# Kernel optimization log

Measured on AMD Instinct MI355X. Metric: run time of the kernel, lower is better.

## Reference

```python
import jax, jax.numpy as jnp
import numpy as np

NUM_CLASSES = 54
EPSILON = 0.001
IMPORTANT = [1, 3, 5, 7, 11, 13, 17, 19, 23, 29, 31, 37]
BATCH = 2_000_000


def setup_inputs() -> dict:
    key = jax.random.key(0)
    k1, k2 = jax.random.split(key)
    logits = jax.random.normal(k1, (BATCH, NUM_CLASSES), dtype=jnp.float32)
    target = jax.random.randint(k2, (BATCH,), 0, NUM_CLASSES, dtype=jnp.int64 if jax.config.read('jax_enable_x64') else jnp.int32)
    important_mask = jnp.zeros((NUM_CLASSES,), dtype=bool).at[jnp.array(IMPORTANT)].set(True)
    return {"logits": logits, "target": target, "important_mask": important_mask}


def reference(logits, target, important_mask):
    # softmax over classes
    sm = jax.nn.softmax(logits, axis=1)                     # [B, C]
    pred = jnp.argmax(sm, axis=1)                           # [B]
    # vectorized membership test (replaces the per-sample .item() loop)
    keep = important_mask[pred] | important_mask[target]    # [B]
    # NLLLoss only reads the target column of log(adjusted_softmax):
    #   kept sample   -> softmax[i, target[i]]
    #   ignored sample-> 1 - (C-1)*epsilon  (constant)
    p_target = jnp.take_along_axis(sm, target[:, None], axis=1)[:, 0]  # [B]
    target_prob = 1.0 - (NUM_CLASSES - 1) * EPSILON
    adj = jnp.where(keep, p_target, target_prob)
    loss = -jnp.mean(jnp.log(adj))
    return loss
```

## Files before the change

### kernel.cpp

```cpp
#include <hip/hip_runtime.h>

#define NCLS 54
#define ROWS 64
#define BATCH_N 2000000
#define NTILES (BATCH_N / ROWS)
#define DATA_FLOATS (ROWS * NCLS)
#define TILE_DWORDS (DATA_FLOATS + ROWS)
#define NBLOCKS 1280

#define IMP_MASK ((1ULL << 1) | (1ULL << 3) | (1ULL << 5) | (1ULL << 7) |   \
                  (1ULL << 11) | (1ULL << 13) | (1ULL << 17) | (1ULL << 19) | \
                  (1ULL << 23) | (1ULL << 29) | (1ULL << 31) | (1ULL << 37))

typedef __attribute__((address_space(3))) unsigned int lds_u32;
typedef const __attribute__((address_space(1))) unsigned int glob_u32;

__global__ __launch_bounds__(64) void loss_main(
    const float* __restrict__ logits,
    const int* __restrict__ target,
    float* __restrict__ partial) {
    __shared__ __align__(16) unsigned int tile[2][TILE_DWORDS];

    const int tid = threadIdx.x;

    auto prefetch = [&](int t, int buf) {
        const glob_u32* g = (const glob_u32*)(logits + (size_t)t * DATA_FLOATS);
#pragma unroll
        for (int c = 0; c < 13; ++c) {
            __builtin_amdgcn_global_load_lds(
                g + c * 256 + tid * 4, (lds_u32*)(&tile[buf][c * 256]), 16, 0, 0);
        }
        if (tid < 32) {
            __builtin_amdgcn_global_load_lds(
                g + 13 * 256 + tid * 4, (lds_u32*)(&tile[buf][13 * 256]), 16, 0, 0);
        }
        const glob_u32* gt = (const glob_u32*)(target + (size_t)t * ROWS);
        if (tid < 16) {
            __builtin_amdgcn_global_load_lds(
                gt + tid * 4, (lds_u32*)(&tile[buf][DATA_FLOATS]), 16, 0, 0);
        }
    };

    int t = blockIdx.x;
    prefetch(t, 0);
    prefetch(t + NBLOCKS, 1);

    float acc = 0.0f;
    int buf = 0;
    for (; t < NTILES; t += NBLOCKS) {
        if (t + NBLOCKS < NTILES) {
            asm volatile("s_waitcnt vmcnt(15)" ::: "memory");
        } else {
            asm volatile("s_waitcnt vmcnt(0)" ::: "memory");
        }

        const float* rv = (const float*)&tile[buf][tid * NCLS];
        float v[NCLS];
#pragma unroll
        for (int j = 0; j < NCLS / 2; ++j) {
            float2 t2 = reinterpret_cast<const float2*>(rv)[j];
            v[2 * j] = t2.x;
            v[2 * j + 1] = t2.y;
        }
        const int tg = ((const int*)&tile[buf][DATA_FLOATS])[tid];
        const float vt = rv[tg];

        asm volatile("s_waitcnt lgkmcnt(0)" ::: "memory");
        if (t + 2 * NBLOCKS < NTILES) prefetch(t + 2 * NBLOCKS, buf);

        float w[27];
#pragma unroll
        for (int j = 0; j < 27; ++j) w[j] = fmaxf(v[j], v[j + 27]);
#pragma unroll
        for (int j = 0; j < 13; ++j) w[j] = fmaxf(w[j], w[j + 14]);
#pragma unroll
        for (int j = 0; j < 7; ++j) w[j] = fmaxf(w[j], w[j + 7]);
#pragma unroll
        for (int j = 0; j < 3; ++j) w[j] = fmaxf(w[j], w[j + 4]);
        w[0] = fmaxf(w[0], w[2]);
        w[1] = fmaxf(w[1], w[3]);
        const float m = fmaxf(w[0], w[1]);

        const int IMP[12] = {1, 3, 5, 7, 11, 13, 17, 19, 23, 29, 31, 37};
        bool imp_pred = false;
#pragma unroll
        for (int j = 0; j < 12; ++j) imp_pred |= (v[IMP[j]] == m);
        const bool keep = imp_pred || (((IMP_MASK >> tg) & 1ULL) != 0ULL);

        float s0 = 0.f, s1 = 0.f, s2 = 0.f, s3 = 0.f;
#pragma unroll
        for (int j = 0; j < 52; j += 4) {
            s0 += __expf(v[j]);
            s1 += __expf(v[j + 1]);
            s2 += __expf(v[j + 2]);
            s3 += __expf(v[j + 3]);
        }
        s0 += __expf(v[52]);
        s1 += __expf(v[53]);
        const float s = (s0 + s1) + (s2 + s3);

        acc += keep ? (__logf(s) - vt) : 0.054456182f;

        buf ^= 1;
    }

#pragma unroll
    for (int off = 32; off > 0; off >>= 1) {
        acc += __shfl_down(acc, off, 64);
    }
    if (tid == 0) partial[blockIdx.x] = acc;
}

__global__ __launch_bounds__(1024) void loss_reduce(
    const float* __restrict__ partial, int n, float* __restrict__ out) {
    float s = 0.f;
    for (int i = threadIdx.x; i < n; i += 1024) s += partial[i];
#pragma unroll
    for (int off = 32; off > 0; off >>= 1) {
        s += __shfl_down(s, off, 64);
    }
    __shared__ float wsum[16];
    int lane = threadIdx.x & 63;
    int wid = threadIdx.x >> 6;
    if (lane == 0) wsum[wid] = s;
    __syncthreads();
    if (threadIdx.x == 0) {
        float bs = 0.f;
#pragma unroll
        for (int k = 0; k < 16; ++k) bs += wsum[k];
        out[0] = bs * (1.0f / (float)BATCH_N);
    }
}

extern "C" void kernel_launch(void* const* d_in, const int* in_sizes, int n_in,
                              void* d_out, int out_size, void* d_ws, size_t ws_size,
                              hipStream_t stream) {
    const float* logits = (const float*)d_in[0];
    const int* target   = (const int*)d_in[1];
    float* out = (float*)d_out;
    float* partial = (float*)d_ws;

    loss_main<<<NBLOCKS, ROWS, 0, stream>>>(logits, target, partial);
    loss_reduce<<<1, 1024, 0, stream>>>(partial, NBLOCKS, out);
}
```

Measured before the change: 558.2 us.

## Replace async global-to-LDS double buffering with register-staged prefetch

Drops the direct global_load_lds double-buffered pipeline and instead loads the next tile into registers (27 float2 per thread), writes them into a single LDS tile, syncs, then issues the next tile's loads while computing. The grid grows from 1280 to 2048 blocks and the kernel gets a minimum-occupancy hint of 2 in launch_bounds. This is meant to simplify the waitcnt handling and raise concurrency through more resident blocks. In exchange it costs extra registers and LDS writes, and the single buffer with no barrier after the compute may race with the next iteration's LDS stores.

Result: no change. 552.9 us (-1.0%).

```diff
diff --git a/kernel.cpp b/kernel.cpp
--- a/kernel.cpp
+++ b/kernel.cpp
@@ -4,57 +4,47 @@
 #define ROWS 64
 #define BATCH_N 2000000
 #define NTILES (BATCH_N / ROWS)
-#define DATA_FLOATS (ROWS * NCLS)
-#define TILE_DWORDS (DATA_FLOATS + ROWS)
-#define NBLOCKS 1280
+#define TILE_FLOATS (ROWS * NCLS)
+#define TILE_F2 (TILE_FLOATS / 2)
+#define NB 2048
 
 #define IMP_MASK ((1ULL << 1) | (1ULL << 3) | (1ULL << 5) | (1ULL << 7) |   \
                   (1ULL << 11) | (1ULL << 13) | (1ULL << 17) | (1ULL << 19) | \
                   (1ULL << 23) | (1ULL << 29) | (1ULL << 31) | (1ULL << 37))
 
-typedef __attribute__((address_space(3))) unsigned int lds_u32;
-typedef const __attribute__((address_space(1))) unsigned int glob_u32;
-
-__global__ __launch_bounds__(64) void loss_main(
+__global__ __launch_bounds__(64, 2) void loss_main(
     const float* __restrict__ logits,
     const int* __restrict__ target,
     float* __restrict__ partial) {
-    __shared__ __align__(16) unsigned int tile[2][TILE_DWORDS];
+    __shared__ __align__(16) float tile[TILE_FLOATS];
 
     const int tid = threadIdx.x;
 
-    auto prefetch = [&](int t, int buf) {
-        const glob_u32* g = (const glob_u32*)(logits + (size_t)t * DATA_FLOATS);
+    float2 st[27];
+    int tg_next;
+
+    auto issue_loads = [&](int tt) {
+        const float2* g = reinterpret_cast<const float2*>(logits) + (size_t)tt * TILE_F2;
 #pragma unroll
-        for (int c = 0; c < 13; ++c) {
-            __builtin_amdgcn_global_load_lds(
-                g + c * 256 + tid * 4, (lds_u32*)(&tile[buf][c * 256]), 16, 0, 0);
-        }
-        if (tid < 32) {
-            __builtin_amdgcn_global_load_lds(
-                g + 13 * 256 + tid * 4, (lds_u32*)(&tile[buf][13 * 256]), 16, 0, 0);
-        }
-        const glob_u32* gt = (const glob_u32*)(target + (size_t)t * ROWS);
-        if (tid < 16) {
-            __builtin_amdgcn_global_load_lds(
-                gt + tid * 4, (lds_u32*)(&tile[buf][DATA_FLOATS]), 16, 0, 0);
-        }
+        for (int i = 0; i < 27; ++i) st[i] = g[i * 64 + tid];
+        tg_next = target[(size_t)tt * ROWS + tid];
     };
 
     int t = blockIdx.x;
-    prefetch(t, 0);
-    prefetch(t + NBLOCKS, 1);
+    issue_loads(t);
 
     float acc = 0.0f;
-    int buf = 0;
-    for (; t < NTILES; t += NBLOCKS) {
-        if (t + NBLOCKS < NTILES) {
-            asm volatile("s_waitcnt vmcnt(15)" ::: "memory");
-        } else {
-            asm volatile("s_waitcnt vmcnt(0)" ::: "memory");
-        }
+    for (; t < NTILES; t += NB) {
+        float2* lds2 = reinterpret_cast<float2*>(tile);
+#pragma unroll
+        for (int i = 0; i < 27; ++i) lds2[i * 64 + tid] = st[i];
 
-        const float* rv = (const float*)&tile[buf][tid * NCLS];
+        const int tg = tg_next;
+        __syncthreads();
+
+        if (t + NB < NTILES) issue_loads(t + NB);
+
+        const float* rv = &tile[tid * NCLS];
         float v[NCLS];
 #pragma unroll
         for (int j = 0; j < NCLS / 2; ++j) {
@@ -62,11 +52,7 @@
             v[2 * j] = t2.x;
             v[2 * j + 1] = t2.y;
         }
-        const int tg = ((const int*)&tile[buf][DATA_FLOATS])[tid];
         const float vt = rv[tg];
-
-        asm volatile("s_waitcnt lgkmcnt(0)" ::: "memory");
-        if (t + 2 * NBLOCKS < NTILES) prefetch(t + 2 * NBLOCKS, buf);
 
         float w[27];
 #pragma unroll
@@ -100,8 +86,6 @@
         const float s = (s0 + s1) + (s2 + s3);
 
         acc += keep ? (__logf(s) - vt) : 0.054456182f;
-
-        buf ^= 1;
     }
 
 #pragma unroll
@@ -140,6 +124,6 @@
     float* out = (float*)d_out;
     float* partial = (float*)d_ws;
 
-    loss_main<<<NBLOCKS, ROWS, 0, stream>>>(logits, target, partial);
-    loss_reduce<<<1, 1024, 0, stream>>>(partial, NBLOCKS, out);
+    loss_main<<<NB, ROWS, 0, stream>>>(logits, target, partial);
+    loss_reduce<<<1, 1024, 0, stream>>>(partial, NB, out);
 }
```
